# Performance work log

Hardware: AMD Instinct MI355X
Metric: run time of the kernel (lower is better)

The kernel has to match this reference:

```python
import jax, jax.numpy as jnp
import numpy as np

B, T, C = 2, 2048, 2048
N_HEAD, N_KV = 16, 2
D_HEAD = C // N_HEAD          # 128
R = N_HEAD // N_KV            # q heads per kv head = 8


def setup_inputs() -> dict:
    key = jax.random.key(0)
    ks = jax.random.split(key, 5)
    s = 0.02
    return {
        "x": jax.random.normal(ks[0], (B, T, C), dtype=jnp.float32),
        "Wq": jax.random.normal(ks[1], (C, C), dtype=jnp.float32) * s,
        "Wk": jax.random.normal(ks[2], (C, N_KV * D_HEAD), dtype=jnp.float32) * s,
        "Wv": jax.random.normal(ks[3], (C, N_KV * D_HEAD), dtype=jnp.float32) * s,
        "Wo": jax.random.normal(ks[4], (C, C), dtype=jnp.float32) * s,
    }


def reference(x, Wq, Wk, Wv, Wo):
    b, t, c = x.shape
    # projections (no bias per config.bias=False)
    q = (x @ Wq).reshape(b, t, N_KV, R, D_HEAD)        # group q heads by kv group
    k = (x @ Wk).reshape(b, t, N_KV, D_HEAD)
    v = (x @ Wv).reshape(b, t, N_KV, D_HEAD)
    scale = 1.0 / jnp.sqrt(jnp.float32(D_HEAD))
    # scores: [b, g(kv), r, tq, tk] -- broadcast kv heads instead of repeat_interleave
    att = jnp.einsum('btgrd,bsgd->bgrts', q, k) * scale
    causal = jnp.tril(jnp.ones((t, t), dtype=bool))
    att = jnp.where(causal, att, -jnp.inf)
    att = jax.nn.softmax(att, axis=-1)
    y = jnp.einsum('bgrts,bsgd->btgrd', att, v).reshape(b, t, c)
    return y @ Wo
```

## Files before the change

kernel.cpp:

```cpp
#include <hip/hip_runtime.h>
#include <stdint.h>

using bf16x8 = __attribute__((ext_vector_type(8))) __bf16;
using f32x4  = __attribute__((ext_vector_type(4))) float;

#define GLL(g, l) __builtin_amdgcn_global_load_lds(                                  \
    (const __attribute__((address_space(1))) void*)(g),                              \
    (__attribute__((address_space(3))) void*)(l), 16, 0, 0)

__device__ __forceinline__ unsigned short f2bf(float f) {
  unsigned u = __builtin_bit_cast(unsigned, f);
  u += 0x7FFF + ((u >> 16) & 1);
  return (unsigned short)(u >> 16);
}
__device__ __forceinline__ float bf2f(unsigned short u) {
  unsigned v = ((unsigned)u) << 16;
  return __builtin_bit_cast(float, v);
}

__global__ __launch_bounds__(256) void cast_kernel(const float* __restrict__ in,
                                                   unsigned short* __restrict__ out, int n4) {
  int i = blockIdx.x * 256 + threadIdx.x;
  if (i >= n4) return;
  float4 v = reinterpret_cast<const float4*>(in)[i];
  ushort4 o;
  o.x = f2bf(v.x); o.y = f2bf(v.y); o.z = f2bf(v.z); o.w = f2bf(v.w);
  reinterpret_cast<ushort4*>(out)[i] = o;
}

__global__ __launch_bounds__(256) void tcast_kernel(const float* __restrict__ W,
                                                    unsigned short* __restrict__ Wt,
                                                    int K, int N) {
  __shared__ float T[64][65];
  const int k0 = blockIdx.x * 64, n0 = blockIdx.y * 64;
  const int t = threadIdx.x;
  const int r4 = t >> 6, c = t & 63;
#pragma unroll
  for (int p = 0; p < 16; ++p) {
    int r = p * 4 + r4;
    T[r][c] = W[(size_t)(k0 + r) * N + n0 + c];
  }
  __syncthreads();
#pragma unroll
  for (int p = 0; p < 16; ++p) {
    int r = p * 4 + r4;
    Wt[(size_t)(n0 + r) * K + k0 + c] = f2bf(T[c][r]);
  }
}

__global__ __launch_bounds__(256) void tv_kernel(const unsigned short* __restrict__ V,
                                                 unsigned short* __restrict__ Vt) {
  __shared__ unsigned short T[64][68];
  const int t0 = blockIdx.x * 64;
  const int d0 = blockIdx.y * 64;
  const int t = threadIdx.x;
  const int r4 = t >> 6, c = t & 63;
#pragma unroll
  for (int p = 0; p < 16; ++p) {
    int r = p * 4 + r4;
    T[r][c] = V[(size_t)(t0 + r) * 2560 + 2304 + d0 + c];
  }
  __syncthreads();
  const int b = t0 >> 11;
  const int tl = t0 & 2047;
#pragma unroll
  for (int p = 0; p < 16; ++p) {
    int dr = p * 4 + r4;
    int dg = d0 + dr;
    int g = dg >> 7, dl = dg & 127;
    Vt[(size_t)((b * 2 + g) * 128 + dl) * 2048 + tl + c] = T[c][dr];
  }
}

template <bool FP32OUT>
__global__ __launch_bounds__(256) void gemm_bt_kernel(const unsigned short* __restrict__ A,
                                                      const unsigned short* __restrict__ Bt,
                                                      void* __restrict__ Cout,
                                                      int K, int lda, int ldb, int ldc,
                                                      float scale, int nscale) {
  __shared__ __align__(16) unsigned short As[128 * 64];
  __shared__ __align__(16) unsigned short Bs[128 * 64];
  const int m0 = blockIdx.x * 128, n0 = blockIdx.y * 128;
  const int t = threadIdx.x;
  const int w = t >> 6, lane = t & 63;
  const int l15 = lane & 15, quad = lane >> 4;
  const int wm = (w >> 1) * 64, wn = (w & 1) * 64;

  const int srow = lane >> 3;
  const int sgl = (lane & 7) ^ srow;

  f32x4 acc[4][4] = {};

  for (int k0 = 0; k0 < K; k0 += 64) {
    __syncthreads();
#pragma unroll
    for (int p = 0; p < 4; ++p) {
      int rowbase = p * 32 + w * 8;
      GLL(&A[(size_t)(m0 + rowbase + srow) * lda + k0 + sgl * 8], &As[rowbase * 64]);
      GLL(&Bt[(size_t)(n0 + rowbase + srow) * ldb + k0 + sgl * 8], &Bs[rowbase * 64]);
    }
    __syncthreads();
#pragma unroll
    for (int kk = 0; kk < 64; kk += 32) {
      const int kg = kk >> 3;
      const int phys = ((kg + quad) ^ (l15 & 7)) * 8;
      bf16x8 af[4], bfr[4];
#pragma unroll
      for (int mt = 0; mt < 4; ++mt)
        af[mt] = *reinterpret_cast<const bf16x8*>(&As[(wm + mt * 16 + l15) * 64 + phys]);
#pragma unroll
      for (int nt = 0; nt < 4; ++nt)
        bfr[nt] = *reinterpret_cast<const bf16x8*>(&Bs[(wn + nt * 16 + l15) * 64 + phys]);
#pragma unroll
      for (int mt = 0; mt < 4; ++mt)
#pragma unroll
        for (int nt = 0; nt < 4; ++nt)
          acc[mt][nt] = __builtin_amdgcn_mfma_f32_16x16x32_bf16(af[mt], bfr[nt], acc[mt][nt], 0, 0, 0);
    }
  }

  const float sc = (n0 < nscale) ? scale : 1.0f;
#pragma unroll
  for (int mt = 0; mt < 4; ++mt) {
#pragma unroll
    for (int reg = 0; reg < 4; ++reg) {
      int row = m0 + wm + mt * 16 + quad * 4 + reg;
#pragma unroll
      for (int nt = 0; nt < 4; ++nt) {
        int col = n0 + wn + nt * 16 + l15;
        float v = acc[mt][nt][reg] * sc;
        if (FP32OUT)
          reinterpret_cast<float*>(Cout)[(size_t)row * ldc + col] = v;
        else
          reinterpret_cast<unsigned short*>(Cout)[(size_t)row * ldc + col] = f2bf(v);
      }
    }
  }
}

#define LDQK 2560
__global__ __launch_bounds__(256, 2) void attn_kernel(const unsigned short* __restrict__ Q,
                                                      const unsigned short* __restrict__ Kg,
                                                      const unsigned short* __restrict__ Vt,
                                                      float* __restrict__ O0,
                                                      unsigned short* __restrict__ O1,
                                                      float* __restrict__ L) {
  __shared__ __align__(16) unsigned short Ks[2][64 * 128];
  __shared__ __align__(16) unsigned short Vs[2][128 * 64];
  __shared__ __align__(16) unsigned short Pw[4][32 * 32];

  const int s  = blockIdx.x;
  const int bx = blockIdx.y;
  const int hh = blockIdx.z & 15;
  const int b  = blockIdx.z >> 4;
  const int g  = hh >> 3;
  const int t  = threadIdx.x;
  const int wg = t >> 6, lane = t & 63;
  const int l15 = lane & 15, quad = lane >> 4;

  const unsigned short* Kbase = Kg + (size_t)b * 2048 * LDQK + g * 128;
  const unsigned short* Vbase = Vt + (size_t)(b * 2 + g) * 128 * 2048;

  const int k_r = lane >> 4;
  const int v_r = lane >> 3;

  auto issueK = [&](int tile, unsigned short* dst) {
    const unsigned short* kb = Kbase + (size_t)(tile * 64) * LDQK;
#pragma unroll
    for (int p = 0; p < 4; ++p) {
      int rowbase = p * 16 + wg * 4;
      int row = rowbase + k_r;
      int gl = (lane & 15) ^ (row & 15);
      GLL(&kb[(size_t)row * LDQK + gl * 8], &dst[rowbase * 128]);
    }
  };
  auto issueV = [&](int tile, unsigned short* dst) {
    const unsigned short* vb = Vbase + tile * 64;
#pragma unroll
    for (int p = 0; p < 4; ++p) {
      int rowbase = p * 32 + wg * 8;
      int row = rowbase + v_r;
      int gl = (lane & 7) ^ (row & 7);
      GLL(&vb[(size_t)row * 2048 + gl * 8], &dst[rowbase * 64]);
    }
  };

  int pb = 0;
  issueK(s, Ks[0]);
  issueV(s, Vs[0]);

  for (int ph = 0; ph < 2; ++ph) {
    const int iq = ph ? (15 - bx) : bx;

    bf16x8 qf[2][4];
#pragma unroll
    for (int mi = 0; mi < 2; ++mi) {
      int qrow = iq * 128 + wg * 32 + mi * 16 + l15;
      const unsigned short* qp = &Q[(size_t)(b * 2048 + qrow) * LDQK + hh * 128 + quad * 8];
#pragma unroll
      for (int dk = 0; dk < 4; ++dk)
        qf[mi][dk] = *reinterpret_cast<const bf16x8*>(qp + dk * 32);
    }

    f32x4 o[2][8] = {};
    float l_run[2][4] = {};

    for (int j = 0; j <= iq; ++j) {
      const int tile = 2 * j + s;
      __syncthreads();
      const int cur = pb, nxt = pb ^ 1;

      if (j < iq) {
        issueK(tile + 2, Ks[nxt]);
        issueV(tile + 2, Vs[nxt]);
      } else if (ph == 0) {
        issueK(s, Ks[nxt]);
        issueV(s, Vs[nxt]);
      }

      f32x4 sc[2][4] = {};
#pragma unroll
      for (int nt = 0; nt < 4; ++nt) {
#pragma unroll
        for (int dk = 0; dk < 4; ++dk) {
          int phys = (dk * 4 + quad) ^ l15;
          bf16x8 kf = *reinterpret_cast<const bf16x8*>(&Ks[cur][(nt * 16 + l15) * 128 + phys * 8]);
          sc[0][nt] = __builtin_amdgcn_mfma_f32_16x16x32_bf16(qf[0][dk], kf, sc[0][nt], 0, 0, 0);
          sc[1][nt] = __builtin_amdgcn_mfma_f32_16x16x32_bf16(qf[1][dk], kf, sc[1][nt], 0, 0, 0);
        }
      }
      if (j == iq) {
#pragma unroll
        for (int mi = 0; mi < 2; ++mi)
#pragma unroll
          for (int nt = 0; nt < 4; ++nt) {
            int kcol = tile * 64 + nt * 16 + l15;
#pragma unroll
            for (int reg = 0; reg < 4; ++reg) {
              int qr = iq * 128 + wg * 32 + mi * 16 + quad * 4 + reg;
              if (kcol > qr) sc[mi][nt][reg] = -1e30f;
            }
          }
      }

#pragma unroll
      for (int kk = 0; kk < 2; ++kk) {
#pragma unroll
        for (int ntl = 0; ntl < 2; ++ntl) {
          const int nt = kk * 2 + ntl;
#pragma unroll
          for (int mi = 0; mi < 2; ++mi)
#pragma unroll
            for (int reg = 0; reg < 4; ++reg) {
              float p = __builtin_exp2f(__builtin_fmaf(sc[mi][nt][reg], 1.44269504f, -23.08312064f));
              l_run[mi][reg] += p;
              int row = mi * 16 + quad * 4 + reg;
              int slot = (ntl * 2 + (l15 >> 3)) ^ (row & 3);
              Pw[wg][row * 32 + slot * 8 + (l15 & 7)] = f2bf(p);
            }
        }
        bf16x8 pf[2];
#pragma unroll
        for (int mi = 0; mi < 2; ++mi) {
          int row = mi * 16 + l15;
          int slot = quad ^ (row & 3);
          pf[mi] = *reinterpret_cast<const bf16x8*>(&Pw[wg][row * 32 + slot * 8]);
        }
#pragma unroll
        for (int dt = 0; dt < 8; ++dt) {
          int phys = ((kk * 4 + quad) ^ (l15 & 7));
          bf16x8 vf = *reinterpret_cast<const bf16x8*>(&Vs[cur][(dt * 16 + l15) * 64 + phys * 8]);
#pragma unroll
          for (int mi = 0; mi < 2; ++mi)
            o[mi][dt] = __builtin_amdgcn_mfma_f32_16x16x32_bf16(pf[mi], vf, o[mi][dt], 0, 0, 0);
        }
      }
      pb ^= 1;
    }

#pragma unroll
    for (int off = 1; off <= 8; off <<= 1)
#pragma unroll
      for (int mi = 0; mi < 2; ++mi)
#pragma unroll
        for (int reg = 0; reg < 4; ++reg)
          l_run[mi][reg] += __shfl_xor(l_run[mi][reg], off);

#pragma unroll
    for (int mi = 0; mi < 2; ++mi)
#pragma unroll
      for (int reg = 0; reg < 4; ++reg) {
        int row = wg * 32 + mi * 16 + quad * 4 + reg;
        size_t base = (size_t)(b * 2048 + iq * 128 + row) * 2048 + hh * 128;
        if (s == 0) {
#pragma unroll
          for (int dt = 0; dt < 8; ++dt)
            O0[base + dt * 16 + l15] = o[mi][dt][reg];
        } else {
#pragma unroll
          for (int dt = 0; dt < 8; ++dt)
            O1[base + dt * 16 + l15] = f2bf(o[mi][dt][reg]);
        }
        if (l15 == 0)
          L[(size_t)s * 65536 + (size_t)(b * 2048 + iq * 128 + row) * 16 + hh] = l_run[mi][reg];
      }
  }
}

__global__ __launch_bounds__(256) void merge_kernel(const float* __restrict__ O0,
                                                    unsigned short* __restrict__ O1,
                                                    const float* __restrict__ L) {
  int i4 = blockIdx.x * 256 + threadIdx.x;
  int e = i4 << 2;
  int tr = e >> 11;
  int hh = (e >> 7) & 15;
  float l = L[tr * 16 + hh] + L[65536 + tr * 16 + hh];
  float inv = 1.0f / l;
  float4 a = reinterpret_cast<const float4*>(O0)[i4];
  ushort4 u = reinterpret_cast<const ushort4*>(O1)[i4];
  ushort4 r;
  r.x = f2bf((a.x + bf2f(u.x)) * inv);
  r.y = f2bf((a.y + bf2f(u.y)) * inv);
  r.z = f2bf((a.z + bf2f(u.z)) * inv);
  r.w = f2bf((a.w + bf2f(u.w)) * inv);
  reinterpret_cast<ushort4*>(O1)[i4] = r;
}

extern "C" void kernel_launch(void* const* d_in, const int* in_sizes, int n_in,
                              void* d_out, int out_size, void* d_ws, size_t ws_size,
                              hipStream_t stream) {
  const float* x  = (const float*)d_in[0];
  const float* Wq = (const float*)d_in[1];
  const float* Wk = (const float*)d_in[2];
  const float* Wv = (const float*)d_in[3];
  const float* Wo = (const float*)d_in[4];

  char* ws = (char*)d_ws;
  unsigned short* xb    = (unsigned short*)(ws + 0);
  unsigned short* Wqkvt = (unsigned short*)(ws + 16777216);
  unsigned short* Wot   = (unsigned short*)(ws + 27262976);
  unsigned short* QKVb  = (unsigned short*)(ws + 35651584);
  unsigned short* Vtb   = (unsigned short*)(ws + 56623104);
  float*          Lb    = (float*)(ws + 58720256);
  unsigned short* Yb    = xb;

  cast_kernel<<<8192, 256, 0, stream>>>(x, xb, 2097152);
  tcast_kernel<<<dim3(32, 32), 256, 0, stream>>>(Wq, Wqkvt, 2048, 2048);
  tcast_kernel<<<dim3(32, 4),  256, 0, stream>>>(Wk, Wqkvt + (size_t)2048 * 2048, 2048, 256);
  tcast_kernel<<<dim3(32, 4),  256, 0, stream>>>(Wv, Wqkvt + (size_t)2304 * 2048, 2048, 256);
  tcast_kernel<<<dim3(32, 32), 256, 0, stream>>>(Wo, Wot, 2048, 2048);

  const float qscale = 0.08838834764831845f;
  gemm_bt_kernel<false><<<dim3(32, 20), 256, 0, stream>>>(xb, Wqkvt, QKVb,
                                                          2048, 2048, 2048, 2560, qscale, 2048);
  tv_kernel<<<dim3(64, 4), 256, 0, stream>>>(QKVb, Vtb);
  attn_kernel<<<dim3(2, 8, 32), 256, 0, stream>>>(QKVb, QKVb + 2048, Vtb,
                                                  (float*)d_out, Yb, Lb);
  merge_kernel<<<8192, 256, 0, stream>>>((const float*)d_out, Yb, Lb);
  gemm_bt_kernel<true><<<dim3(32, 16), 256, 0, stream>>>(Yb, Wot, d_out,
                                                         2048, 2048, 2048, 2048, 1.0f, 0);
}
```

Before: 286.7 us.

## Halve attention tile sizes for higher occupancy and merge weight transpose launches

Attention tiles shrink to 64 query rows (16 per wave) and 32-key tiles, with smaller LDS buffers and launch bounds raised to 4 blocks per SM, so twice as many blocks are launched for better occupancy and load balance. The P staging layout is simplified to a padded row stride instead of an XOR swizzle. Separately, the four weight transpose-cast launches are fused into one kernel that picks its source by blockIdx.y, cutting launch overhead. Smaller tiles mean more K/V reloads per query row and more barriers per unit of work.

```diff
diff --git a/kernel.cpp b/kernel.cpp
--- a/kernel.cpp
+++ b/kernel.cpp
@@ -28,11 +28,22 @@
   reinterpret_cast<ushort4*>(out)[i] = o;
 }
 
-__global__ __launch_bounds__(256) void tcast_kernel(const float* __restrict__ W,
-                                                    unsigned short* __restrict__ Wt,
-                                                    int K, int N) {
+__global__ __launch_bounds__(256) void tcast_all_kernel(const float* __restrict__ Wq,
+                                                        const float* __restrict__ Wk,
+                                                        const float* __restrict__ Wv,
+                                                        const float* __restrict__ Wo,
+                                                        unsigned short* __restrict__ Wqkvt,
+                                                        unsigned short* __restrict__ Wot) {
   __shared__ float T[64][65];
-  const int k0 = blockIdx.x * 64, n0 = blockIdx.y * 64;
+  const int y = blockIdx.y;
+  const float* W;
+  unsigned short* Wt;
+  int N, n0;
+  if (y < 32)      { W = Wq; Wt = Wqkvt;                          N = 2048; n0 = y * 64; }
+  else if (y < 36) { W = Wk; Wt = Wqkvt + (size_t)2048 * 2048;    N = 256;  n0 = (y - 32) * 64; }
+  else if (y < 40) { W = Wv; Wt = Wqkvt + (size_t)2304 * 2048;    N = 256;  n0 = (y - 36) * 64; }
+  else             { W = Wo; Wt = Wot;                            N = 2048; n0 = (y - 40) * 64; }
+  const int k0 = blockIdx.x * 64;
   const int t = threadIdx.x;
   const int r4 = t >> 6, c = t & 63;
 #pragma unroll
@@ -44,7 +55,7 @@
 #pragma unroll
   for (int p = 0; p < 16; ++p) {
     int r = p * 4 + r4;
-    Wt[(size_t)(n0 + r) * K + k0 + c] = f2bf(T[c][r]);
+    Wt[(size_t)(n0 + r) * 2048 + k0 + c] = f2bf(T[c][r]);
   }
 }
 
@@ -139,18 +150,18 @@
 }
 
 #define LDQK 2560
-__global__ __launch_bounds__(256, 2) void attn_kernel(const unsigned short* __restrict__ Q,
+__global__ __launch_bounds__(256, 4) void attn_kernel(const unsigned short* __restrict__ Q,
                                                       const unsigned short* __restrict__ Kg,
                                                       const unsigned short* __restrict__ Vt,
                                                       float* __restrict__ O0,
                                                       unsigned short* __restrict__ O1,
                                                       float* __restrict__ L) {
-  __shared__ __align__(16) unsigned short Ks[2][64 * 128];
-  __shared__ __align__(16) unsigned short Vs[2][128 * 64];
-  __shared__ __align__(16) unsigned short Pw[4][32 * 32];
+  __shared__ __align__(16) unsigned short Ks[2][32 * 128];
+  __shared__ __align__(16) unsigned short Vs[2][128 * 32];
+  __shared__ __align__(16) unsigned short Pw[4][16 * 40];
 
   const int s  = blockIdx.x;
-  const int bx = blockIdx.y;
+  const int by = blockIdx.y;
   const int hh = blockIdx.z & 15;
   const int b  = blockIdx.z >> 4;
   const int g  = hh >> 3;
@@ -162,118 +173,99 @@
   const unsigned short* Vbase = Vt + (size_t)(b * 2 + g) * 128 * 2048;
 
   const int k_r = lane >> 4;
-  const int v_r = lane >> 3;
-
-  auto issueK = [&](int tile, unsigned short* dst) {
-    const unsigned short* kb = Kbase + (size_t)(tile * 64) * LDQK;
-#pragma unroll
-    for (int p = 0; p < 4; ++p) {
+  const int k_g = lane & 15;
+  const int v_r = lane >> 2;
+  const int v_g = lane & 3;
+
+  auto issueK = [&](int tile, int buf) {
+    const unsigned short* kb = Kbase + (size_t)(tile * 32) * LDQK;
+#pragma unroll
+    for (int p = 0; p < 2; ++p) {
       int rowbase = p * 16 + wg * 4;
       int row = rowbase + k_r;
-      int gl = (lane & 15) ^ (row & 15);
-      GLL(&kb[(size_t)row * LDQK + gl * 8], &dst[rowbase * 128]);
+      int gl = k_g ^ (row & 15);
+      GLL(&kb[(size_t)row * LDQK + gl * 8], &Ks[buf][rowbase * 128]);
     }
   };
-  auto issueV = [&](int tile, unsigned short* dst) {
-    const unsigned short* vb = Vbase + tile * 64;
-#pragma unroll
-    for (int p = 0; p < 4; ++p) {
-      int rowbase = p * 32 + wg * 8;
+  auto issueV = [&](int tile, int buf) {
+    const unsigned short* vb = Vbase + tile * 32;
+#pragma unroll
+    for (int p = 0; p < 2; ++p) {
+      int rowbase = p * 64 + wg * 16;
       int row = rowbase + v_r;
-      int gl = (lane & 7) ^ (row & 7);
-      GLL(&vb[(size_t)row * 2048 + gl * 8], &dst[rowbase * 64]);
+      int gl = v_g ^ (row & 3);
+      GLL(&vb[(size_t)row * 2048 + gl * 8], &Vs[buf][rowbase * 32]);
     }
   };
 
   int pb = 0;
-  issueK(s, Ks[0]);
-  issueV(s, Vs[0]);
+  issueK(s, 0);
+  issueV(s, 0);
 
   for (int ph = 0; ph < 2; ++ph) {
-    const int iq = ph ? (15 - bx) : bx;
-
-    bf16x8 qf[2][4];
-#pragma unroll
-    for (int mi = 0; mi < 2; ++mi) {
-      int qrow = iq * 128 + wg * 32 + mi * 16 + l15;
+    const int qt = ph ? (31 - by) : by;
+
+    bf16x8 qf[4];
+    {
+      int qrow = qt * 64 + wg * 16 + l15;
       const unsigned short* qp = &Q[(size_t)(b * 2048 + qrow) * LDQK + hh * 128 + quad * 8];
 #pragma unroll
       for (int dk = 0; dk < 4; ++dk)
-        qf[mi][dk] = *reinterpret_cast<const bf16x8*>(qp + dk * 32);
-    }
-
-    f32x4 o[2][8] = {};
-    float l_run[2][4] = {};
-
-    for (int j = 0; j <= iq; ++j) {
+        qf[dk] = *reinterpret_cast<const bf16x8*>(qp + dk * 32);
+    }
+
+    f32x4 o[8] = {};
+    float l_run[4] = {};
+
+    for (int j = 0; j <= qt; ++j) {
       const int tile = 2 * j + s;
       __syncthreads();
       const int cur = pb, nxt = pb ^ 1;
 
-      if (j < iq) {
-        issueK(tile + 2, Ks[nxt]);
-        issueV(tile + 2, Vs[nxt]);
+      if (j < qt) {
+        issueK(tile + 2, nxt);
+        issueV(tile + 2, nxt);
       } else if (ph == 0) {
-        issueK(s, Ks[nxt]);
-        issueV(s, Vs[nxt]);
-      }
-
-      f32x4 sc[2][4] = {};
-#pragma unroll
-      for (int nt = 0; nt < 4; ++nt) {
+        issueK(s, nxt);
+        issueV(s, nxt);
+      }
+
+      f32x4 sc[2] = {};
+#pragma unroll
+      for (int nt = 0; nt < 2; ++nt) {
 #pragma unroll
         for (int dk = 0; dk < 4; ++dk) {
           int phys = (dk * 4 + quad) ^ l15;
           bf16x8 kf = *reinterpret_cast<const bf16x8*>(&Ks[cur][(nt * 16 + l15) * 128 + phys * 8]);
-          sc[0][nt] = __builtin_amdgcn_mfma_f32_16x16x32_bf16(qf[0][dk], kf, sc[0][nt], 0, 0, 0);
-          sc[1][nt] = __builtin_amdgcn_mfma_f32_16x16x32_bf16(qf[1][dk], kf, sc[1][nt], 0, 0, 0);
+          sc[nt] = __builtin_amdgcn_mfma_f32_16x16x32_bf16(qf[dk], kf, sc[nt], 0, 0, 0);
         }
       }
-      if (j == iq) {
-#pragma unroll
-        for (int mi = 0; mi < 2; ++mi)
-#pragma unroll
-          for (int nt = 0; nt < 4; ++nt) {
-            int kcol = tile * 64 + nt * 16 + l15;
-#pragma unroll
-            for (int reg = 0; reg < 4; ++reg) {
-              int qr = iq * 128 + wg * 32 + mi * 16 + quad * 4 + reg;
-              if (kcol > qr) sc[mi][nt][reg] = -1e30f;
-            }
+      if (j == qt) {
+#pragma unroll
+        for (int nt = 0; nt < 2; ++nt) {
+          int kcol = tile * 32 + nt * 16 + l15;
+#pragma unroll
+          for (int reg = 0; reg < 4; ++reg) {
+            int qr = qt * 64 + wg * 16 + quad * 4 + reg;
+            if (kcol > qr) sc[nt][reg] = -1e30f;
           }
-      }
-
-#pragma unroll
-      for (int kk = 0; kk < 2; ++kk) {
-#pragma unroll
-        for (int ntl = 0; ntl < 2; ++ntl) {
-          const int nt = kk * 2 + ntl;
-#pragma unroll
-          for (int mi = 0; mi < 2; ++mi)
-#pragma unroll
-            for (int reg = 0; reg < 4; ++reg) {
-              float p = __builtin_exp2f(__builtin_fmaf(sc[mi][nt][reg], 1.44269504f, -23.08312064f));
-              l_run[mi][reg] += p;
-              int row = mi * 16 + quad * 4 + reg;
-              int slot = (ntl * 2 + (l15 >> 3)) ^ (row & 3);
-              Pw[wg][row * 32 + slot * 8 + (l15 & 7)] = f2bf(p);
-            }
         }
-        bf16x8 pf[2];
-#pragma unroll
-        for (int mi = 0; mi < 2; ++mi) {
-          int row = mi * 16 + l15;
-          int slot = quad ^ (row & 3);
-          pf[mi] = *reinterpret_cast<const bf16x8*>(&Pw[wg][row * 32 + slot * 8]);
+      }
+#pragma unroll
+      for (int nt = 0; nt < 2; ++nt)
+#pragma unroll
+        for (int reg = 0; reg < 4; ++reg) {
+          float p = __builtin_exp2f(__builtin_fmaf(sc[nt][reg], 1.44269504f, -23.08312064f));
+          l_run[reg] += p;
+          Pw[wg][(quad * 4 + reg) * 40 + nt * 16 + l15] = f2bf(p);
         }
-#pragma unroll
-        for (int dt = 0; dt < 8; ++dt) {
-          int phys = ((kk * 4 + quad) ^ (l15 & 7));
-          bf16x8 vf = *reinterpret_cast<const bf16x8*>(&Vs[cur][(dt * 16 + l15) * 64 + phys * 8]);
-#pragma unroll
-          for (int mi = 0; mi < 2; ++mi)
-            o[mi][dt] = __builtin_amdgcn_mfma_f32_16x16x32_bf16(pf[mi], vf, o[mi][dt], 0, 0, 0);
-        }
+
+      bf16x8 pf = *reinterpret_cast<const bf16x8*>(&Pw[wg][l15 * 40 + quad * 8]);
+#pragma unroll
+      for (int dt = 0; dt < 8; ++dt) {
+        int phys = quad ^ (l15 & 3);
+        bf16x8 vf = *reinterpret_cast<const bf16x8*>(&Vs[cur][(dt * 16 + l15) * 32 + phys * 8]);
+        o[dt] = __builtin_amdgcn_mfma_f32_16x16x32_bf16(pf, vf, o[dt], 0, 0, 0);
       }
       pb ^= 1;
     }
@@ -281,29 +273,25 @@
 #pragma unroll
     for (int off = 1; off <= 8; off <<= 1)
 #pragma unroll
-      for (int mi = 0; mi < 2; ++mi)
-#pragma unroll
-        for (int reg = 0; reg < 4; ++reg)
-          l_run[mi][reg] += __shfl_xor(l_run[mi][reg], off);
-
-#pragma unroll
-    for (int mi = 0; mi < 2; ++mi)
-#pragma unroll
-      for (int reg = 0; reg < 4; ++reg) {
-        int row = wg * 32 + mi * 16 + quad * 4 + reg;
-        size_t base = (size_t)(b * 2048 + iq * 128 + row) * 2048 + hh * 128;
-        if (s == 0) {
-#pragma unroll
-          for (int dt = 0; dt < 8; ++dt)
-            O0[base + dt * 16 + l15] = o[mi][dt][reg];
-        } else {
-#pragma unroll
-          for (int dt = 0; dt < 8; ++dt)
-            O1[base + dt * 16 + l15] = f2bf(o[mi][dt][reg]);
-        }
-        if (l15 == 0)
-          L[(size_t)s * 65536 + (size_t)(b * 2048 + iq * 128 + row) * 16 + hh] = l_run[mi][reg];
-      }
+      for (int reg = 0; reg < 4; ++reg)
+        l_run[reg] += __shfl_xor(l_run[reg], off);
+
+#pragma unroll
+    for (int reg = 0; reg < 4; ++reg) {
+      int row = wg * 16 + quad * 4 + reg;
+      size_t base = (size_t)(b * 2048 + qt * 64 + row) * 2048 + hh * 128;
+      if (s == 0) {
+#pragma unroll
+        for (int dt = 0; dt < 8; ++dt)
+          O0[base + dt * 16 + l15] = o[dt][reg];
+      } else {
+#pragma unroll
+        for (int dt = 0; dt < 8; ++dt)
+          O1[base + dt * 16 + l15] = f2bf(o[dt][reg]);
+      }
+      if (l15 == 0)
+        L[(size_t)s * 65536 + (size_t)(b * 2048 + qt * 64 + row) * 16 + hh] = l_run[reg];
+    }
   }
 }
 
@@ -345,17 +333,14 @@
   unsigned short* Yb    = xb;
 
   cast_kernel<<<8192, 256, 0, stream>>>(x, xb, 2097152);
-  tcast_kernel<<<dim3(32, 32), 256, 0, stream>>>(Wq, Wqkvt, 2048, 2048);
-  tcast_kernel<<<dim3(32, 4),  256, 0, stream>>>(Wk, Wqkvt + (size_t)2048 * 2048, 2048, 256);
-  tcast_kernel<<<dim3(32, 4),  256, 0, stream>>>(Wv, Wqkvt + (size_t)2304 * 2048, 2048, 256);
-  tcast_kernel<<<dim3(32, 32), 256, 0, stream>>>(Wo, Wot, 2048, 2048);
+  tcast_all_kernel<<<dim3(32, 72), 256, 0, stream>>>(Wq, Wk, Wv, Wo, Wqkvt, Wot);
 
   const float qscale = 0.08838834764831845f;
   gemm_bt_kernel<false><<<dim3(32, 20), 256, 0, stream>>>(xb, Wqkvt, QKVb,
                                                           2048, 2048, 2048, 2560, qscale, 2048);
   tv_kernel<<<dim3(64, 4), 256, 0, stream>>>(QKVb, Vtb);
-  attn_kernel<<<dim3(2, 8, 32), 256, 0, stream>>>(QKVb, QKVb + 2048, Vtb,
-                                                  (float*)d_out, Yb, Lb);
+  attn_kernel<<<dim3(2, 16, 32), 256, 0, stream>>>(QKVb, QKVb + 2048, Vtb,
+                                                   (float*)d_out, Yb, Lb);
   merge_kernel<<<8192, 256, 0, stream>>>((const float*)d_out, Yb, Lb);
   gemm_bt_kernel<true><<<dim3(32, 16), 256, 0, stream>>>(Yb, Wot, d_out,
                                                          2048, 2048, 2048, 2048, 1.0f, 0);
```

New measurement: 288.3 us. About the same (+0.6%).
